# Kernel tuning notes

Hardware: AMD Instinct MI355X
Metric: run time of the kernel (lower is better)

Reference implementation:

```python
import jax, jax.numpy as jnp
import numpy as np

N, T, E, V = 262144, 1024, 8, 1  # samples, table size, edge_size, vector dim


def setup_inputs() -> dict:
    key = jax.random.key(0)
    k1, k2, k3, k4 = jax.random.split(key, 4)
    inputs = jax.random.normal(k1, (N, 1), jnp.float32) * 2.0
    # quantization grid: sorted values spanning the input range
    evaluate_table = jnp.sort(jax.random.normal(k2, (T, 1), jnp.float32) * 2.0, axis=0)
    # positive inverse-temperature per table entry
    takecare_table = jax.random.uniform(k3, (T, 1), jnp.float32, minval=1.0, maxval=10.0)
    vector_table = jax.random.normal(k4, (T, V), jnp.float32)
    return {
        "inputs": inputs,
        "evaluate_table": evaluate_table,
        "takecare_table": takecare_table,
        "vector_table": vector_table,
        "edge_size": E,
    }


def reference(inputs, evaluate_table, takecare_table, vector_table, edge_size):
    table_len = evaluate_table.shape[0]
    idx_min, idx_max = edge_size, table_len - edge_size - 1
    x = inputs[..., None]                                  # (N,1,1)
    # full distance tensor against the lookup table -> nearest entry
    dist = (x - evaluate_table[None]) ** 2                 # (N,T,1)
    idx = jnp.argmin(dist, axis=-2)                        # (N,1) int
    takecare = takecare_table[idx]                         # (N,1,1)
    offsets = jnp.arange(-edge_size, edge_size + 1)        # (2E+1,)
    win = jnp.clip(idx, idx_min, idx_max) + offsets[None]  # (N,2E+1)
    evaluate = evaluate_table[win]                         # (N,2E+1,1)
    vector = vector_table[win]                             # (N,2E+1,V)
    # local softmax over the window, sharpened by takecare
    score = jax.nn.softmax(-((x - evaluate) ** 2) * takecare, axis=-2)  # (N,2E+1,1)
    return jnp.sum(vector * score, axis=-2)                # (N,V)
```

## Files before the change

kernel.cpp:

```cpp
#include <hip/hip_runtime.h>


constexpr int T_SIZE = 1024;
constexpr int E_SIZE = 8;
constexpr int WIN    = 2 * E_SIZE + 1;
constexpr int BLOCK  = 256;
constexpr int T_PAD  = T_SIZE + (T_SIZE >> 5);

__device__ __forceinline__ float hwnet_finish(
    float x, int lo,
    const float2* __restrict__ s_ev,
    const float* __restrict__ s_take)
{
    int idx;
    if (lo == 0) {
        idx = 0;
    } else if (lo == T_SIZE) {
        idx = T_SIZE - 1;
    } else {
        const float d0 = x - s_ev[lo - 1].x;
        const float d1 = x - s_ev[lo].x;
        idx = (d0 * d0 <= d1 * d1) ? (lo - 1) : lo;
    }
    while (idx > 0) {
        const float dp = x - s_ev[idx - 1].x;
        const float dc = x - s_ev[idx].x;
        if (dp * dp <= dc * dc) --idx; else break;
    }

    const float take = s_take[idx];

    int c = idx;
    if (c < E_SIZE) c = E_SIZE;
    if (c > T_SIZE - 1 - E_SIZE) c = T_SIZE - 1 - E_SIZE;
    const int base = c - E_SIZE;

    float sum = 0.0f, acc = 0.0f;
    #pragma unroll
    for (int k = 0; k < WIN; ++k) {
        const float2 ev = s_ev[base + k];
        const float d = x - ev.x;
        const float e = __expf(-(d * d) * take);
        sum += e;
        acc += e * ev.y;
    }
    return acc / sum;
}

__global__ __launch_bounds__(BLOCK) void hwnet_kernel(
    const float* __restrict__ inputs,
    const float* __restrict__ eval_t,
    const float* __restrict__ take_t,
    const float* __restrict__ vec_t,
    float* __restrict__ out,
    int n)
{
    __shared__ float  s_evs[T_PAD];
    __shared__ float2 s_ev[T_SIZE];
    __shared__ float  s_take[T_SIZE];

    {
        const int i4 = threadIdx.x * 4;
        const float4 e4 = *reinterpret_cast<const float4*>(eval_t + i4);
        const float4 t4 = *reinterpret_cast<const float4*>(take_t + i4);
        const float4 v4 = *reinterpret_cast<const float4*>(vec_t + i4);
        const float ee[4] = {e4.x, e4.y, e4.z, e4.w};
        const float tt[4] = {t4.x, t4.y, t4.z, t4.w};
        const float vv[4] = {v4.x, v4.y, v4.z, v4.w};
        #pragma unroll
        for (int k = 0; k < 4; ++k) {
            const int i = i4 + k;
            s_evs[i + (i >> 5)] = ee[k];
            s_ev[i] = make_float2(ee[k], vv[k]);
            s_take[i] = tt[k];
        }
    }
    __syncthreads();

    const int gid2 = blockIdx.x * BLOCK + threadIdx.x;
    const int n2 = n >> 1;
    if (gid2 < n2) {
        const float2 x2 = reinterpret_cast<const float2*>(inputs)[gid2];

        int lo0 = 0, hi0 = T_SIZE, lo1 = 0, hi1 = T_SIZE;
        #pragma unroll
        for (int it = 0; it < 10; ++it) {
            const int m0 = (lo0 + hi0) >> 1;
            const int m1 = (lo1 + hi1) >> 1;
            const float e0 = s_evs[m0 + (m0 >> 5)];
            const float e1 = s_evs[m1 + (m1 >> 5)];
            if (e0 < x2.x) lo0 = m0 + 1; else hi0 = m0;
            if (e1 < x2.y) lo1 = m1 + 1; else hi1 = m1;
        }

        const float r0 = hwnet_finish(x2.x, lo0, s_ev, s_take);
        const float r1 = hwnet_finish(x2.y, lo1, s_ev, s_take);
        reinterpret_cast<float2*>(out)[gid2] = make_float2(r0, r1);
    }

    if ((n & 1) && gid2 == 0) {
        const float x = inputs[n - 1];
        int lo = 0, hi = T_SIZE;
        for (int it = 0; it < 10; ++it) {
            const int mid = (lo + hi) >> 1;
            if (s_evs[mid + (mid >> 5)] < x) lo = mid + 1; else hi = mid;
        }
        out[n - 1] = hwnet_finish(x, lo, s_ev, s_take);
    }
}

extern "C" void kernel_launch(void* const* d_in, const int* in_sizes, int n_in,
                              void* d_out, int out_size, void* d_ws, size_t ws_size,
                              hipStream_t stream) {
    const float* inputs = (const float*)d_in[0];
    const float* eval_t = (const float*)d_in[1];
    const float* take_t = (const float*)d_in[2];
    const float* vec_t  = (const float*)d_in[3];
    float* out = (float*)d_out;

    const int n = in_sizes[0];
    const int n2 = n >> 1;
    const int grid = (n2 + BLOCK - 1) / BLOCK;
    hwnet_kernel<<<grid, BLOCK, 0, stream>>>(inputs, eval_t, take_t, vec_t, out, n);
}
```

Before: 11.07 us.

## Replace binary search with three-level counting search over register and LDS pivots

Swaps the 10-step dependent binary search in shared memory for a three-level branchless count. The first level compares against 31 pivots held in registers and loaded per thread from global memory. The second compares 7 sub-pivots in LDS, and the last reads one float4 from LDS. This shortens the chain of dependent LDS reads, at the cost of more compares, higher register pressure and 31 extra global loads per thread.

```diff
diff --git a/kernel.cpp b/kernel.cpp
--- a/kernel.cpp
+++ b/kernel.cpp
@@ -5,7 +5,6 @@
 constexpr int E_SIZE = 8;
 constexpr int WIN    = 2 * E_SIZE + 1;
 constexpr int BLOCK  = 256;
-constexpr int T_PAD  = T_SIZE + (T_SIZE >> 5);
 
 __device__ __forceinline__ float hwnet_finish(
     float x, int lo,
@@ -55,22 +54,26 @@
     float* __restrict__ out,
     int n)
 {
-    __shared__ float  s_evs[T_PAD];
+    __shared__ alignas(16) float s_evf[T_SIZE];
     __shared__ float2 s_ev[T_SIZE];
     __shared__ float  s_take[T_SIZE];
+
+    float pA[31];
+    #pragma unroll
+    for (int k = 0; k < 31; ++k) pA[k] = eval_t[(k + 1) << 5];
 
     {
         const int i4 = threadIdx.x * 4;
         const float4 e4 = *reinterpret_cast<const float4*>(eval_t + i4);
         const float4 t4 = *reinterpret_cast<const float4*>(take_t + i4);
         const float4 v4 = *reinterpret_cast<const float4*>(vec_t + i4);
+        *reinterpret_cast<float4*>(s_evf + i4) = e4;
         const float ee[4] = {e4.x, e4.y, e4.z, e4.w};
         const float tt[4] = {t4.x, t4.y, t4.z, t4.w};
         const float vv[4] = {v4.x, v4.y, v4.z, v4.w};
         #pragma unroll
         for (int k = 0; k < 4; ++k) {
             const int i = i4 + k;
-            s_evs[i + (i >> 5)] = ee[k];
             s_ev[i] = make_float2(ee[k], vv[k]);
             s_take[i] = tt[k];
         }
@@ -82,16 +85,35 @@
     if (gid2 < n2) {
         const float2 x2 = reinterpret_cast<const float2*>(inputs)[gid2];
 
-        int lo0 = 0, hi0 = T_SIZE, lo1 = 0, hi1 = T_SIZE;
+        int c0 = 0, c1 = 0;
         #pragma unroll
-        for (int it = 0; it < 10; ++it) {
-            const int m0 = (lo0 + hi0) >> 1;
-            const int m1 = (lo1 + hi1) >> 1;
-            const float e0 = s_evs[m0 + (m0 >> 5)];
-            const float e1 = s_evs[m1 + (m1 >> 5)];
-            if (e0 < x2.x) lo0 = m0 + 1; else hi0 = m0;
-            if (e1 < x2.y) lo1 = m1 + 1; else hi1 = m1;
+        for (int k = 0; k < 31; ++k) {
+            c0 += (pA[k] < x2.x) ? 1 : 0;
+            c1 += (pA[k] < x2.y) ? 1 : 0;
         }
+        int b0 = c0 << 5, b1 = c1 << 5;
+
+        float qb0[7], qb1[7];
+        #pragma unroll
+        for (int k = 0; k < 7; ++k) {
+            qb0[k] = s_evf[b0 + ((k + 1) << 2)];
+            qb1[k] = s_evf[b1 + ((k + 1) << 2)];
+        }
+        int d0 = 0, d1 = 0;
+        #pragma unroll
+        for (int k = 0; k < 7; ++k) {
+            d0 += (qb0[k] < x2.x) ? 1 : 0;
+            d1 += (qb1[k] < x2.y) ? 1 : 0;
+        }
+        b0 += d0 << 2;
+        b1 += d1 << 2;
+
+        const float4 q0 = *reinterpret_cast<const float4*>(s_evf + b0);
+        const float4 q1 = *reinterpret_cast<const float4*>(s_evf + b1);
+        const int lo0 = b0 + ((q0.x < x2.x) ? 1 : 0) + ((q0.y < x2.x) ? 1 : 0)
+                           + ((q0.z < x2.x) ? 1 : 0) + ((q0.w < x2.x) ? 1 : 0);
+        const int lo1 = b1 + ((q1.x < x2.y) ? 1 : 0) + ((q1.y < x2.y) ? 1 : 0)
+                           + ((q1.z < x2.y) ? 1 : 0) + ((q1.w < x2.y) ? 1 : 0);
 
         const float r0 = hwnet_finish(x2.x, lo0, s_ev, s_take);
         const float r1 = hwnet_finish(x2.y, lo1, s_ev, s_take);
@@ -103,7 +125,7 @@
         int lo = 0, hi = T_SIZE;
         for (int it = 0; it < 10; ++it) {
             const int mid = (lo + hi) >> 1;
-            if (s_evs[mid + (mid >> 5)] < x) lo = mid + 1; else hi = mid;
+            if (s_evf[mid] < x) lo = mid + 1; else hi = mid;
         }
         out[n - 1] = hwnet_finish(x, lo, s_ev, s_take);
     }
```

After: 11.38 us. +2.8%, slower.
